# Optimization experiments

Hardware: AMD Instinct MI355X
Metric: run time of the kernel (lower is better)

The kernel has to match this reference:

```python
import jax, jax.numpy as jnp
import numpy as np

NUM_LOC = 20000
T = 24
IN_DIM = 18
H1 = 32
H2 = 32
GRU = 32
PW = 15
E_RAND = 640000


def setup_inputs() -> dict:
    key = jax.random.key(0)
    ks = jax.random.split(key, 32)
    # graph: random edges + self loops so every node has >=1 incoming edge
    edge_src = jnp.concatenate([
        jax.random.randint(ks[0], (E_RAND,), 0, NUM_LOC),
        jnp.arange(NUM_LOC)]).astype(jnp.int32)
    edge_dst = jnp.concatenate([
        jax.random.randint(ks[1], (E_RAND,), 0, NUM_LOC),
        jnp.arange(NUM_LOC)]).astype(jnp.int32)
    dynamic = jax.random.normal(ks[2], (NUM_LOC, T, IN_DIM), dtype=jnp.float32)
    cI = jax.random.uniform(ks[3], (T,), dtype=jnp.float32)
    cR = jax.random.uniform(ks[4], (T,), dtype=jnp.float32)
    I = jax.random.uniform(ks[5], (T,), dtype=jnp.float32)
    R = jax.random.uniform(ks[6], (T,), dtype=jnp.float32)
    N = jax.random.uniform(ks[7], (NUM_LOC, 1), dtype=jnp.float32) * 1e4 + 10.0
    h0 = jax.random.normal(ks[8], (1, GRU), dtype=jnp.float32) * 0.1
    s = 0.1
    # GAT layer 1 (torch Linear convention: weight [out, in], y = x @ W.T + b)
    W1 = jax.random.normal(ks[9], (H1, IN_DIM), dtype=jnp.float32) * s
    b1 = jnp.zeros((H1,), dtype=jnp.float32)
    aW1 = jax.random.normal(ks[10], (1, 2 * H1), dtype=jnp.float32) * s
    ab1 = jnp.zeros((1,), dtype=jnp.float32)
    # GAT layer 2
    W2 = jax.random.normal(ks[11], (H2, H1), dtype=jnp.float32) * s
    b2 = jnp.zeros((H2,), dtype=jnp.float32)
    aW2 = jax.random.normal(ks[12], (1, 2 * H2), dtype=jnp.float32) * s
    ab2 = jnp.zeros((1,), dtype=jnp.float32)
    # GRUCell
    Wih = jax.random.normal(ks[13], (3 * GRU, H2), dtype=jnp.float32) * s
    Whh = jax.random.normal(ks[14], (3 * GRU, GRU), dtype=jnp.float32) * s
    bih = jnp.zeros((3 * GRU,), dtype=jnp.float32)
    bhh = jnp.zeros((3 * GRU,), dtype=jnp.float32)
    # output heads
    WI = jax.random.normal(ks[15], (PW, GRU + 2), dtype=jnp.float32) * s
    bI = jnp.zeros((PW,), dtype=jnp.float32)
    WR = jax.random.normal(ks[16], (PW, GRU + 2), dtype=jnp.float32) * s
    bR = jnp.zeros((PW,), dtype=jnp.float32)
    Ws = jax.random.normal(ks[17], (2, GRU + 2), dtype=jnp.float32) * s
    bs = jnp.zeros((2,), dtype=jnp.float32)
    return {"dynamic": dynamic, "cI": cI, "cR": cR, "N": N, "I": I, "R": R,
            "h0": h0, "W1": W1, "b1": b1, "aW1": aW1, "ab1": ab1,
            "W2": W2, "b2": b2, "aW2": aW2, "ab2": ab2,
            "Wih": Wih, "Whh": Whh, "bih": bih, "bhh": bhh,
            "WI": WI, "bI": bI, "WR": WR, "bR": bR, "Ws": Ws, "bs": bs,
            "edge_src": edge_src, "edge_dst": edge_dst}


def _gat(x, W, b, aW, ab, src, dst):
    # z = fc(x); per-edge attention e = leaky_relu(attn_fc([z_src, z_dst]))
    z = x @ W.T + b                                        # [n, out]
    e = jax.nn.leaky_relu(
        (jnp.concatenate([z[src], z[dst]], axis=1) @ aW.T + ab)[:, 0])  # [E]
    # softmax over incoming edges per destination node
    m = jax.ops.segment_max(e, dst, num_segments=NUM_LOC)
    ex = jnp.exp(e - m[dst])
    den = jax.ops.segment_sum(ex, dst, num_segments=NUM_LOC)
    alpha = ex / den[dst]
    return jax.ops.segment_sum(alpha[:, None] * z[src], dst, num_segments=NUM_LOC)


def reference(dynamic, cI, cR, N, I, R, h0,
              W1, b1, aW1, ab1, W2, b2, aW2, ab2,
              Wih, Whh, bih, bhh, WI, bI, WR, bR, Ws, bs,
              edge_src, edge_dst):
    Nv = N[:, 0]                                          # [num_loc]

    def step(h, inp):
        x_t, cI_t, cR_t, I_t, R_t = inp
        c = jax.nn.elu(_gat(x_t, W1, b1, aW1, ab1, edge_src, edge_dst))
        c = jax.nn.elu(_gat(c, W2, b2, aW2, ab2, edge_src, edge_dst))
        pooled = jnp.max(c, axis=0)[None, :]              # [1, H2]
        # GRUCell
        gi = pooled @ Wih.T + bih
        gh = h @ Whh.T + bhh
        r = jax.nn.sigmoid(gi[:, :GRU] + gh[:, :GRU])
        zg = jax.nn.sigmoid(gi[:, GRU:2 * GRU] + gh[:, GRU:2 * GRU])
        n = jnp.tanh(gi[:, 2 * GRU:] + r * gh[:, 2 * GRU:])
        h_new = (1.0 - zg) * n + zg * h                   # [1, GRU]
        hc = jnp.concatenate([h_new, cI_t.reshape(1, 1), cR_t.reshape(1, 1)], axis=1)
        pred_I = hc @ WI.T + bI                           # [1, PW]
        pred_R = hc @ WR.T + bR
        sir = hc @ Ws.T + bs                              # [1, 2]
        alpha = jax.nn.sigmoid(sir[0, 0])
        beta = jax.nn.sigmoid(sir[0, 1])

        def sir_step(carry, _):
            lI, lR = carry
            lS = Nv - lI - lR
            dI = alpha * lI * (lS / Nv) - beta * lI
            dR = beta * lI
            return (lI + jax.lax.stop_gradient(dI),
                    lR + jax.lax.stop_gradient(dR)), (dI, dR)

        init = (jnp.broadcast_to(I_t, Nv.shape), jnp.broadcast_to(R_t, Nv.shape))
        _, (dIs, dRs) = jax.lax.scan(sir_step, init, None, length=PW)
        # [PW, num_loc] -> [num_loc, PW]
        return h_new, (pred_I, pred_R, dIs.T, dRs.T)

    xs = (jnp.swapaxes(dynamic, 0, 1), cI, cR, I, R)      # time-major
    h_fin, (nI, nR, pI, pR) = jax.lax.scan(step, h0, xs)
    new_I = jnp.transpose(nI, (1, 0, 2))                  # [1, T, PW]
    new_R = jnp.transpose(nR, (1, 0, 2))
    phy_I = jnp.transpose(pI, (1, 0, 2))                  # [num_loc, T, PW]
    phy_R = jnp.transpose(pR, (1, 0, 2))
    return new_I, new_R, phy_I, phy_R, h_fin
```

## Files before the change

kernel.cpp:

```cpp
#include <hip/hip_runtime.h>
#include <hip/hip_fp16.h>
#include <math.h>
#include <float.h>
#include <type_traits>

#define NLOC 20000
#define TT   24
#define INDIM 18
#define HH   32
#define PWN  15
#define PSTR 32

typedef unsigned short u16;

__device__ __forceinline__ unsigned int fkey(float f) {
    unsigned int b = __float_as_uint(f);
    return b ^ ((unsigned int)((int)b >> 31) | 0x80000000u);
}
__device__ __forceinline__ float funkey(unsigned int u) {
    return (u & 0x80000000u) ? __uint_as_float(u ^ 0x80000000u) : __uint_as_float(~u);
}

__device__ __forceinline__ void decode_t(int nblk, int swz, int tadd,
                                         int& t, int& blk, int& slice) {
    if (swz) {
        int F = blockIdx.x;
        int k = F & 7;
        int g = F >> 3;
        t = k + 8 * (g / nblk);
        blk = g % nblk;
        slice = t;
    } else {
        slice = blockIdx.y;
        t = tadd + slice;
        blk = blockIdx.x;
    }
}

__global__ void count_kernel(const int* __restrict__ dst, int* __restrict__ cnt, int E) {
    int e = blockIdx.x * blockDim.x + threadIdx.x;
    if (e < E) atomicAdd(&cnt[dst[e]], 1);
}

__global__ void scan_kernel(const int* __restrict__ cnt, int* __restrict__ row_ptr, int n) {
    __shared__ int sums[1024];
    const int CH = 20;
    int tid = threadIdx.x;
    int base = tid * CH;
    int local[CH];
    int s = 0;
    #pragma unroll
    for (int i = 0; i < CH; ++i) {
        int idx = base + i;
        int v = (idx < n) ? cnt[idx] : 0;
        local[i] = s;
        s += v;
    }
    sums[tid] = s;
    __syncthreads();
    for (int o = 1; o < 1024; o <<= 1) {
        int v = (tid >= o) ? sums[tid - o] : 0;
        __syncthreads();
        sums[tid] += v;
        __syncthreads();
    }
    int pre = (tid > 0) ? sums[tid - 1] : 0;
    #pragma unroll
    for (int i = 0; i < CH; ++i) {
        int idx = base + i;
        if (idx < n) row_ptr[idx] = pre + local[i];
    }
    if (tid == 1023) row_ptr[n] = sums[1023];
}

__global__ void scatter_kernel(const int* __restrict__ src, const int* __restrict__ dst,
                               const int* __restrict__ row_ptr, int* __restrict__ fill,
                               u16* __restrict__ csr_src, int E) {
    int e = blockIdx.x * blockDim.x + threadIdx.x;
    if (e < E) {
        int d = dst[e];
        int pos = row_ptr[d] + atomicAdd(&fill[d], 1);
        csr_src[pos] = (u16)src[e];
    }
}

template<int IN, bool XABS, typename TIN>
__global__ void node_kernel(const TIN* __restrict__ xbase, long nstride, long tstride,
                            const float* __restrict__ W, const float* __restrict__ b,
                            const float* __restrict__ aW, const float* __restrict__ ab,
                            __half* __restrict__ z, float* __restrict__ es, float* __restrict__ ed,
                            int nblk, int swz, int tadd) {
    __shared__ float sW[HH * IN];
    __shared__ float sb[HH];
    __shared__ float saW[2 * HH];
    __shared__ float sab;
    int t, blk, slice;
    decode_t(nblk, swz, tadd, t, blk, slice);
    int tid = threadIdx.x;
    for (int i = tid; i < HH * IN; i += blockDim.x) sW[i] = W[i];
    if (tid < HH) sb[tid] = b[tid];
    if (tid < 2 * HH) saW[tid] = aW[tid];
    if (tid == 0) sab = ab[0];
    __syncthreads();
    int n = blk * blockDim.x + tid;
    if (n >= NLOC) return;
    z  += (size_t)slice * NLOC * HH;
    es += (size_t)slice * NLOC;
    ed += (size_t)slice * NLOC;
    long xoff = XABS ? (long)t * tstride : (long)slice * tstride;
    const TIN* xp = xbase + (long)n * nstride + xoff;
    float xr[IN];
    if constexpr (std::is_same<TIN, __half>::value) {
        const __half2* hp = (const __half2*)xp;
        #pragma unroll
        for (int i = 0; i < IN / 2; ++i) {
            float2 f = __half22float2(hp[i]);
            xr[2 * i] = f.x; xr[2 * i + 1] = f.y;
        }
    } else {
        #pragma unroll
        for (int i = 0; i < IN; ++i) xr[i] = (float)xp[i];
    }
    float e_s = 0.f, e_d = sab;
    #pragma unroll
    for (int k = 0; k < HH; ++k) {
        float acc = sb[k];
        #pragma unroll
        for (int i = 0; i < IN; ++i) acc = fmaf(xr[i], sW[k * IN + i], acc);
        z[n * HH + k] = __float2half_rn(acc);
        e_s = fmaf(saW[k], acc, e_s);
        e_d = fmaf(saW[HH + k], acc, e_d);
    }
    es[n] = e_s;
    ed[n] = e_d;
}

template<bool WRITE_C, bool POOL>
__global__ void __launch_bounds__(256, 4)
agg_kernel(const int* __restrict__ row_ptr, const u16* __restrict__ csr,
           const __half* __restrict__ zt, const float* __restrict__ es,
           const float* __restrict__ ed, __half* __restrict__ cout,
           unsigned int* __restrict__ pooled_u, int nblk, int swz, int tadd) {
    __shared__ int2  shp[4][64];
    __shared__ float sred[4][HH];
    int t, dblk, slice;
    decode_t(nblk, swz, tadd, t, dblk, slice);
    int lane = threadIdx.x & 63;
    int w    = threadIdx.x >> 6;
    int r    = lane >> 3;
    int cg   = lane & 7;
    int d = dblk * 4 + w;
    const __half* z   = zt + (size_t)slice * NLOC * HH;
    const float*  est = es + (size_t)slice * NLOC;
    const float*  edt = ed + (size_t)slice * NLOC;

    int beg = 0, end = 0;
    float edd = 0.f;
    if (d < NLOC) {
        beg = row_ptr[d];
        end = row_ptr[d + 1];
        edd = edt[d];
    }
    int deg = end - beg;
    int il = beg + lane;
    bool valid = (il < end);
    int idx_l = valid ? (int)csr[il] : 0;
    float ev = est[idx_l] + edd;
    ev = (ev > 0.f) ? ev : 0.01f * ev;
    float w_l = valid ? __expf(ev) : 0.f;
    shp[w][lane] = make_int2(idx_l, __float_as_int(w_l));
    __syncthreads();

    float a0 = 0.f, a1 = 0.f, a2 = 0.f, a3 = 0.f, sden = 0.f;
    #pragma unroll
    for (int pass = 0; pass < 8; ++pass) {
        int2 pw = shp[w][pass * 8 + r];
        float we = __int_as_float(pw.y);
        const __half2* zp = (const __half2*)(z + (size_t)pw.x * HH + cg * 4);
        __half2 h01 = zp[0], h23 = zp[1];
        sden += we;
        a0 = fmaf(we, __half2float(__low2half(h01)),  a0);
        a1 = fmaf(we, __half2float(__high2half(h01)), a1);
        a2 = fmaf(we, __half2float(__low2half(h23)),  a2);
        a3 = fmaf(we, __half2float(__high2half(h23)), a3);
    }
    for (int e = 64 + r; e < deg; e += 8) {
        int s2 = (int)csr[beg + e];
        float ee = est[s2] + edd;
        ee = (ee > 0.f) ? ee : 0.01f * ee;
        float xx = __expf(ee);
        sden += xx;
        const __half2* zp = (const __half2*)(z + (size_t)s2 * HH + cg * 4);
        __half2 h01 = zp[0], h23 = zp[1];
        a0 = fmaf(xx, __half2float(__low2half(h01)),  a0);
        a1 = fmaf(xx, __half2float(__high2half(h01)), a1);
        a2 = fmaf(xx, __half2float(__low2half(h23)),  a2);
        a3 = fmaf(xx, __half2float(__high2half(h23)), a3);
    }
    #pragma unroll
    for (int o = 8; o <= 32; o <<= 1) {
        a0 += __shfl_xor(a0, o, 64);
        a1 += __shfl_xor(a1, o, 64);
        a2 += __shfl_xor(a2, o, 64);
        a3 += __shfl_xor(a3, o, 64);
        sden += __shfl_xor(sden, o, 64);
    }

    float v0 = -FLT_MAX, v1 = -FLT_MAX, v2 = -FLT_MAX, v3 = -FLT_MAX;
    if (d < NLOC) {
        float rden = 1.f / sden;
        v0 = a0 * rden; v0 = (v0 > 0.f) ? v0 : __expf(v0) - 1.f;
        v1 = a1 * rden; v1 = (v1 > 0.f) ? v1 : __expf(v1) - 1.f;
        v2 = a2 * rden; v2 = (v2 > 0.f) ? v2 : __expf(v2) - 1.f;
        v3 = a3 * rden; v3 = (v3 > 0.f) ? v3 : __expf(v3) - 1.f;
        if (WRITE_C && r == 0) {
            __half2 o01 = __floats2half2_rn(v0, v1);
            __half2 o23 = __floats2half2_rn(v2, v3);
            uint2 pk;
            pk.x = *(unsigned int*)&o01;
            pk.y = *(unsigned int*)&o23;
            *(uint2*)&cout[(size_t)slice * NLOC * HH + (size_t)d * HH + cg * 4] = pk;
        }
    }
    if (POOL) {
        if (r == 0) {
            sred[w][cg * 4 + 0] = v0;
            sred[w][cg * 4 + 1] = v1;
            sred[w][cg * 4 + 2] = v2;
            sred[w][cg * 4 + 3] = v3;
        }
        __syncthreads();
        if (threadIdx.x < HH) {
            float m = fmaxf(fmaxf(sred[0][threadIdx.x], sred[1][threadIdx.x]),
                            fmaxf(sred[2][threadIdx.x], sred[3][threadIdx.x]));
            atomicMax(&pooled_u[(size_t)(t * HH + threadIdx.x) * PSTR], fkey(m));
        }
    }
}

__global__ void gru_all_kernel(const unsigned int* __restrict__ pooled_u,
                               const float* __restrict__ Wih, const float* __restrict__ Whh,
                               const float* __restrict__ bih, const float* __restrict__ bhh,
                               const float* __restrict__ WI, const float* __restrict__ bI,
                               const float* __restrict__ WR, const float* __restrict__ bR,
                               const float* __restrict__ Ws, const float* __restrict__ bs,
                               const float* __restrict__ cIv, const float* __restrict__ cRv,
                               const float* __restrict__ h0, float* __restrict__ abArr,
                               float* __restrict__ out_newI, float* __restrict__ out_newR,
                               float* __restrict__ h_fin) {
    __shared__ float pooled[HH], hs[HH], gi[96], gh[96], hc[34];
    int tid = threadIdx.x;
    float wih_r[HH], whh_r[HH];
    if (tid < 96) {
        #pragma unroll
        for (int k = 0; k < HH; ++k) {
            wih_r[k] = Wih[tid * HH + k];
            whh_r[k] = Whh[tid * HH + k];
        }
    }
    if (tid < HH) hs[tid] = h0[tid];
    __syncthreads();
    for (int t = 0; t < TT; ++t) {
        if (tid < HH) pooled[tid] = funkey(pooled_u[(size_t)(t * HH + tid) * PSTR]);
        __syncthreads();
        if (tid < 96) {
            float a = bih[tid], g = bhh[tid];
            #pragma unroll
            for (int k = 0; k < HH; ++k) {
                a = fmaf(wih_r[k], pooled[k], a);
                g = fmaf(whh_r[k], hs[k], g);
            }
            gi[tid] = a; gh[tid] = g;
        }
        __syncthreads();
        if (tid < HH) {
            float r  = 1.f / (1.f + expf(-(gi[tid] + gh[tid])));
            float zg = 1.f / (1.f + expf(-(gi[HH + tid] + gh[HH + tid])));
            float nn = tanhf(gi[2 * HH + tid] + r * gh[2 * HH + tid]);
            float hn = (1.f - zg) * nn + zg * hs[tid];
            hs[tid] = hn;
            hc[tid] = hn;
        }
        if (tid == 32) hc[32] = cIv[t];
        if (tid == 33) hc[33] = cRv[t];
        __syncthreads();
        if (tid < PWN) {
            float a = bI[tid];
            #pragma unroll
            for (int k = 0; k < 34; ++k) a = fmaf(WI[tid * 34 + k], hc[k], a);
            out_newI[t * PWN + tid] = a;
        } else if (tid >= 32 && tid < 32 + PWN) {
            int p = tid - 32;
            float a = bR[p];
            #pragma unroll
            for (int k = 0; k < 34; ++k) a = fmaf(WR[p * 34 + k], hc[k], a);
            out_newR[t * PWN + p] = a;
        } else if (tid == 64 || tid == 65) {
            int p = tid - 64;
            float a = bs[p];
            #pragma unroll
            for (int k = 0; k < 34; ++k) a = fmaf(Ws[p * 34 + k], hc[k], a);
            abArr[2 * t + p] = 1.f / (1.f + expf(-a));
        }
        __syncthreads();
    }
    if (tid < HH) h_fin[tid] = hs[tid];
}

__global__ void sir_kernel(const float* __restrict__ Nin, const float* __restrict__ Iv,
                           const float* __restrict__ Rv, const float* __restrict__ abArr,
                           float* __restrict__ phyI, float* __restrict__ phyR) {
    int idx = blockIdx.x * blockDim.x + threadIdx.x;
    if (idx >= NLOC * TT) return;
    int n = idx / TT, t = idx - n * TT;
    float Nv = Nin[n];
    float alpha = abArr[2 * t], beta = abArr[2 * t + 1];
    float lI = Iv[t], lR = Rv[t];
    float* oI = phyI + (size_t)idx * PWN;
    float* oR = phyR + (size_t)idx * PWN;
    #pragma unroll
    for (int p = 0; p < PWN; ++p) {
        float lS = Nv - lI - lR;
        float dI = alpha * lI * (lS / Nv) - beta * lI;
        float dR = beta * lI;
        oI[p] = dI;
        oR[p] = dR;
        lI += dI;
        lR += dR;
    }
}

extern "C" void kernel_launch(void* const* d_in, const int* in_sizes, int n_in,
                              void* d_out, int out_size, void* d_ws, size_t ws_size,
                              hipStream_t stream) {
    const float* dynamic = (const float*)d_in[0];
    const float* cIv = (const float*)d_in[1];
    const float* cRv = (const float*)d_in[2];
    const float* Nin = (const float*)d_in[3];
    const float* Iv  = (const float*)d_in[4];
    const float* Rv  = (const float*)d_in[5];
    const float* h0  = (const float*)d_in[6];
    const float* W1  = (const float*)d_in[7];
    const float* b1  = (const float*)d_in[8];
    const float* aW1 = (const float*)d_in[9];
    const float* ab1 = (const float*)d_in[10];
    const float* W2  = (const float*)d_in[11];
    const float* b2  = (const float*)d_in[12];
    const float* aW2 = (const float*)d_in[13];
    const float* ab2 = (const float*)d_in[14];
    const float* Wih = (const float*)d_in[15];
    const float* Whh = (const float*)d_in[16];
    const float* bih = (const float*)d_in[17];
    const float* bhh = (const float*)d_in[18];
    const float* WI  = (const float*)d_in[19];
    const float* bI  = (const float*)d_in[20];
    const float* WR  = (const float*)d_in[21];
    const float* bR  = (const float*)d_in[22];
    const float* Ws  = (const float*)d_in[23];
    const float* bs  = (const float*)d_in[24];
    const int* esrc  = (const int*)d_in[25];
    const int* edst  = (const int*)d_in[26];
    const int E = in_sizes[25];

    float* out = (float*)d_out;
    float* out_newI = out;
    float* out_newR = out + TT * PWN;
    float* phyI = out + 2 * TT * PWN;
    float* phyR = phyI + (size_t)NLOC * TT * PWN;
    float* h_fin = phyR + (size_t)NLOC * TT * PWN;

    char* p = (char*)d_ws;
    int* cnt = (int*)p;                 p += (size_t)NLOC * 4;
    int* fill = (int*)p;                p += (size_t)NLOC * 4;
    int* row_ptr = (int*)p;             p += (size_t)(NLOC + 2) * 4;
    u16* csr = (u16*)p;                 p += ((size_t)E * 2 + 15) & ~(size_t)15;
    unsigned int* pooled_u = (unsigned int*)p; p += (size_t)TT * HH * PSTR * 4;
    float* abArr = (float*)p;           p += (size_t)2 * TT * 4;
    p = (char*)(((size_t)p + 15) & ~(size_t)15);
    size_t fixed_bytes = (size_t)(p - (char*)d_ws);
    size_t per_t_bytes = (size_t)(2 * NLOC * HH * 2 + 2 * NLOC * 4);
    int B = 1;
    if (ws_size > fixed_bytes + per_t_bytes)
        B = (int)((ws_size - fixed_bytes) / per_t_bytes);
    if (B > TT) B = TT;
    if (B < 1) B = 1;
    __half* zb  = (__half*)p;
    __half* cb  = zb + (size_t)B * NLOC * HH;
    float* esb  = (float*)(cb + (size_t)B * NLOC * HH);
    float* edb  = esb + (size_t)B * NLOC;

    hipMemsetAsync(cnt, 0, (size_t)2 * NLOC * 4, stream);
    hipMemsetAsync(pooled_u, 0, (size_t)TT * HH * PSTR * 4, stream);

    int egrid = (E + 255) / 256;
    count_kernel<<<egrid, 256, 0, stream>>>(edst, cnt, E);
    scan_kernel<<<1, 1024, 0, stream>>>(cnt, row_ptr, NLOC);
    scatter_kernel<<<egrid, 256, 0, stream>>>(esrc, edst, row_ptr, fill, csr, E);

    const int NBLK_N = (NLOC + 255) / 256;
    const int NBLK_A = (NLOC + 3) / 4;

    if (B >= TT) {
        dim3 ng(NBLK_N * TT), ag(NBLK_A * TT);
        node_kernel<INDIM, true, float><<<ng, 256, 0, stream>>>(
            dynamic, (long)TT * INDIM, (long)INDIM, W1, b1, aW1, ab1,
            zb, esb, edb, NBLK_N, 1, 0);
        agg_kernel<true, false><<<ag, 256, 0, stream>>>(
            row_ptr, csr, zb, esb, edb, cb, pooled_u, NBLK_A, 1, 0);
        node_kernel<HH, false, __half><<<ng, 256, 0, stream>>>(
            cb, (long)HH, (long)NLOC * HH, W2, b2, aW2, ab2,
            zb, esb, edb, NBLK_N, 1, 0);
        agg_kernel<false, true><<<ag, 256, 0, stream>>>(
            row_ptr, csr, zb, esb, edb, nullptr, pooled_u, NBLK_A, 1, 0);
    } else {
        for (int tbase = 0; tbase < TT; tbase += B) {
            int Bc = TT - tbase; if (Bc > B) Bc = B;
            dim3 ng(NBLK_N, Bc), ag(NBLK_A, Bc);
            node_kernel<INDIM, true, float><<<ng, 256, 0, stream>>>(
                dynamic, (long)TT * INDIM, (long)INDIM, W1, b1, aW1, ab1,
                zb, esb, edb, NBLK_N, 0, tbase);
            agg_kernel<true, false><<<ag, 256, 0, stream>>>(
                row_ptr, csr, zb, esb, edb, cb, pooled_u, NBLK_A, 0, tbase);
            node_kernel<HH, false, __half><<<ng, 256, 0, stream>>>(
                cb, (long)HH, (long)NLOC * HH, W2, b2, aW2, ab2,
                zb, esb, edb, NBLK_N, 0, tbase);
            agg_kernel<false, true><<<ag, 256, 0, stream>>>(
                row_ptr, csr, zb, esb, edb, nullptr, pooled_u, NBLK_A, 0, tbase);
        }
    }

    gru_all_kernel<<<1, 128, 0, stream>>>(pooled_u, Wih, Whh, bih, bhh,
                                          WI, bI, WR, bR, Ws, bs, cIv, cRv,
                                          h0, abArr, out_newI, out_newR, h_fin);
    sir_kernel<<<(NLOC * TT + 255) / 256, 256, 0, stream>>>(Nin, Iv, Rv, abArr, phyI, phyR);
}
```

Measured before the change: 706.7 us.

## Interleave timestep pairs in feature layout so each gather serves two timesteps

Node features, attention scores and layer-1 outputs are now stored as pairs of timesteps interleaved (half2 per feature, float2 per score), so each graph edge gather loads 16 bytes covering two timesteps and the CSR index and row lookups are shared across both. The grid covers 12 timestep pairs instead of 24 timesteps, which halves index and row-pointer traffic and halves the number of aggregation blocks. The cost is more registers per thread and a 16-wide swizzle grid of which 4 groups exit immediately. The ELU and LeakyReLU activations are also rewritten in branchless form.

Result: faster. 637.8 us (-9.8%).

```diff
diff --git a/kernel.cpp b/kernel.cpp
--- a/kernel.cpp
+++ b/kernel.cpp
@@ -2,10 +2,10 @@
 #include <hip/hip_fp16.h>
 #include <math.h>
 #include <float.h>
-#include <type_traits>
 
 #define NLOC 20000
 #define TT   24
+#define NP   12
 #define INDIM 18
 #define HH   32
 #define PWN  15
@@ -21,20 +21,18 @@
     return (u & 0x80000000u) ? __uint_as_float(u ^ 0x80000000u) : __uint_as_float(~u);
 }
 
-__device__ __forceinline__ void decode_t(int nblk, int swz, int tadd,
-                                         int& t, int& blk, int& slice) {
+__device__ __forceinline__ bool decode_q(int nblk, int swz, int qadd,
+                                         int& q, int& blk) {
     if (swz) {
         int F = blockIdx.x;
-        int k = F & 7;
         int g = F >> 3;
-        t = k + 8 * (g / nblk);
+        q = (F & 7) + 8 * (g / nblk);
         blk = g % nblk;
-        slice = t;
-    } else {
-        slice = blockIdx.y;
-        t = tadd + slice;
-        blk = blockIdx.x;
-    }
+        return q < NP;
+    }
+    q = qadd + blockIdx.y;
+    blk = blockIdx.x;
+    return true;
 }
 
 __global__ void count_kernel(const int* __restrict__ dst, int* __restrict__ cnt, int E) {
@@ -84,156 +82,220 @@
     }
 }
 
-template<int IN, bool XABS, typename TIN>
-__global__ void node_kernel(const TIN* __restrict__ xbase, long nstride, long tstride,
-                            const float* __restrict__ W, const float* __restrict__ b,
-                            const float* __restrict__ aW, const float* __restrict__ ab,
-                            __half* __restrict__ z, float* __restrict__ es, float* __restrict__ ed,
-                            int nblk, int swz, int tadd) {
-    __shared__ float sW[HH * IN];
+__global__ void node1_kernel(const float* __restrict__ dyn,
+                             const float* __restrict__ W, const float* __restrict__ b,
+                             const float* __restrict__ aW, const float* __restrict__ ab,
+                             __half2* __restrict__ z2, float2* __restrict__ es2,
+                             float2* __restrict__ ed2, int nblk, int swz, int qadd) {
+    __shared__ float sW[HH * INDIM];
     __shared__ float sb[HH];
     __shared__ float saW[2 * HH];
     __shared__ float sab;
-    int t, blk, slice;
-    decode_t(nblk, swz, tadd, t, blk, slice);
+    int q, blk;
+    if (!decode_q(nblk, swz, qadd, q, blk)) return;
+    int slice = swz ? q : blockIdx.y;
     int tid = threadIdx.x;
-    for (int i = tid; i < HH * IN; i += blockDim.x) sW[i] = W[i];
+    for (int i = tid; i < HH * INDIM; i += blockDim.x) sW[i] = W[i];
     if (tid < HH) sb[tid] = b[tid];
     if (tid < 2 * HH) saW[tid] = aW[tid];
     if (tid == 0) sab = ab[0];
     __syncthreads();
     int n = blk * blockDim.x + tid;
     if (n >= NLOC) return;
-    z  += (size_t)slice * NLOC * HH;
-    es += (size_t)slice * NLOC;
-    ed += (size_t)slice * NLOC;
-    long xoff = XABS ? (long)t * tstride : (long)slice * tstride;
-    const TIN* xp = xbase + (long)n * nstride + xoff;
-    float xr[IN];
-    if constexpr (std::is_same<TIN, __half>::value) {
-        const __half2* hp = (const __half2*)xp;
+    z2  += (size_t)slice * NLOC * HH;
+    es2 += (size_t)slice * NLOC;
+    ed2 += (size_t)slice * NLOC;
+    const float* xp = dyn + (size_t)n * (TT * INDIM) + (size_t)(2 * q) * INDIM;
+    float x0[INDIM], x1[INDIM];
+    #pragma unroll
+    for (int i = 0; i < INDIM; ++i) { x0[i] = xp[i]; x1[i] = xp[INDIM + i]; }
+    float es0 = 0.f, es1 = 0.f, ed0 = sab, ed1 = sab;
+    #pragma unroll
+    for (int k = 0; k < HH; ++k) {
+        float a0 = sb[k], a1 = sb[k];
         #pragma unroll
-        for (int i = 0; i < IN / 2; ++i) {
-            float2 f = __half22float2(hp[i]);
-            xr[2 * i] = f.x; xr[2 * i + 1] = f.y;
-        }
-    } else {
+        for (int i = 0; i < INDIM; ++i) {
+            a0 = fmaf(x0[i], sW[k * INDIM + i], a0);
+            a1 = fmaf(x1[i], sW[k * INDIM + i], a1);
+        }
+        z2[(size_t)n * HH + k] = __floats2half2_rn(a0, a1);
+        es0 = fmaf(saW[k], a0, es0);       es1 = fmaf(saW[k], a1, es1);
+        ed0 = fmaf(saW[HH + k], a0, ed0);  ed1 = fmaf(saW[HH + k], a1, ed1);
+    }
+    es2[n] = make_float2(es0, es1);
+    ed2[n] = make_float2(ed0, ed1);
+}
+
+__global__ void node2_kernel(const __half2* __restrict__ c2,
+                             const float* __restrict__ W, const float* __restrict__ b,
+                             const float* __restrict__ aW, const float* __restrict__ ab,
+                             __half2* __restrict__ z2, float2* __restrict__ es2,
+                             float2* __restrict__ ed2, int nblk, int swz, int qadd) {
+    __shared__ float sW[HH * HH];
+    __shared__ float sb[HH];
+    __shared__ float saW[2 * HH];
+    __shared__ float sab;
+    int q, blk;
+    if (!decode_q(nblk, swz, qadd, q, blk)) return;
+    int slice = swz ? q : blockIdx.y;
+    int tid = threadIdx.x;
+    for (int i = tid; i < HH * HH; i += blockDim.x) sW[i] = W[i];
+    if (tid < HH) sb[tid] = b[tid];
+    if (tid < 2 * HH) saW[tid] = aW[tid];
+    if (tid == 0) sab = ab[0];
+    __syncthreads();
+    int n = blk * blockDim.x + tid;
+    if (n >= NLOC) return;
+    c2  += (size_t)slice * NLOC * HH;
+    z2  += (size_t)slice * NLOC * HH;
+    es2 += (size_t)slice * NLOC;
+    ed2 += (size_t)slice * NLOC;
+    float x0[HH], x1[HH];
+    const __half2* cp = c2 + (size_t)n * HH;
+    #pragma unroll
+    for (int i = 0; i < HH; ++i) {
+        float2 f = __half22float2(cp[i]);
+        x0[i] = f.x; x1[i] = f.y;
+    }
+    float es0 = 0.f, es1 = 0.f, ed0 = sab, ed1 = sab;
+    #pragma unroll
+    for (int k = 0; k < HH; ++k) {
+        float a0 = sb[k], a1 = sb[k];
         #pragma unroll
-        for (int i = 0; i < IN; ++i) xr[i] = (float)xp[i];
-    }
-    float e_s = 0.f, e_d = sab;
-    #pragma unroll
-    for (int k = 0; k < HH; ++k) {
-        float acc = sb[k];
-        #pragma unroll
-        for (int i = 0; i < IN; ++i) acc = fmaf(xr[i], sW[k * IN + i], acc);
-        z[n * HH + k] = __float2half_rn(acc);
-        e_s = fmaf(saW[k], acc, e_s);
-        e_d = fmaf(saW[HH + k], acc, e_d);
-    }
-    es[n] = e_s;
-    ed[n] = e_d;
+        for (int i = 0; i < HH; ++i) {
+            a0 = fmaf(x0[i], sW[k * HH + i], a0);
+            a1 = fmaf(x1[i], sW[k * HH + i], a1);
+        }
+        z2[(size_t)n * HH + k] = __floats2half2_rn(a0, a1);
+        es0 = fmaf(saW[k], a0, es0);       es1 = fmaf(saW[k], a1, es1);
+        ed0 = fmaf(saW[HH + k], a0, ed0);  ed1 = fmaf(saW[HH + k], a1, ed1);
+    }
+    es2[n] = make_float2(es0, es1);
+    ed2[n] = make_float2(ed0, ed1);
 }
 
 template<bool WRITE_C, bool POOL>
 __global__ void __launch_bounds__(256, 4)
 agg_kernel(const int* __restrict__ row_ptr, const u16* __restrict__ csr,
-           const __half* __restrict__ zt, const float* __restrict__ es,
-           const float* __restrict__ ed, __half* __restrict__ cout,
-           unsigned int* __restrict__ pooled_u, int nblk, int swz, int tadd) {
-    __shared__ int2  shp[4][64];
-    __shared__ float sred[4][HH];
-    int t, dblk, slice;
-    decode_t(nblk, swz, tadd, t, dblk, slice);
+           const __half2* __restrict__ z2t, const float2* __restrict__ es2,
+           const float2* __restrict__ ed2, __half2* __restrict__ c2out,
+           unsigned int* __restrict__ pooled_u, int nblk, int swz, int qadd) {
+    __shared__ int    soff[4][64];
+    __shared__ float2 swt[4][64];
+    __shared__ float  sred[4][2][HH];
+    int q, dblk;
+    if (!decode_q(nblk, swz, qadd, q, dblk)) return;
+    int slice = swz ? q : blockIdx.y;
     int lane = threadIdx.x & 63;
     int w    = threadIdx.x >> 6;
     int r    = lane >> 3;
     int cg   = lane & 7;
     int d = dblk * 4 + w;
-    const __half* z   = zt + (size_t)slice * NLOC * HH;
-    const float*  est = es + (size_t)slice * NLOC;
-    const float*  edt = ed + (size_t)slice * NLOC;
+    const __half2* z2q  = z2t + (size_t)slice * NLOC * HH;
+    const float2*  es2q = es2 + (size_t)slice * NLOC;
+    const float2*  ed2q = ed2 + (size_t)slice * NLOC;
 
     int beg = 0, end = 0;
-    float edd = 0.f;
+    float edd0 = 0.f, edd1 = 0.f;
     if (d < NLOC) {
         beg = row_ptr[d];
         end = row_ptr[d + 1];
-        edd = edt[d];
+        float2 ev = ed2q[d];
+        edd0 = ev.x; edd1 = ev.y;
     }
     int deg = end - beg;
     int il = beg + lane;
     bool valid = (il < end);
     int idx_l = valid ? (int)csr[il] : 0;
-    float ev = est[idx_l] + edd;
-    ev = (ev > 0.f) ? ev : 0.01f * ev;
-    float w_l = valid ? __expf(ev) : 0.f;
-    shp[w][lane] = make_int2(idx_l, __float_as_int(w_l));
-    __syncthreads();
-
-    float a0 = 0.f, a1 = 0.f, a2 = 0.f, a3 = 0.f, sden = 0.f;
+    float2 esv = es2q[idx_l];
+    float e0 = esv.x + edd0; e0 = fmaxf(e0, 0.01f * e0);
+    float e1 = esv.y + edd1; e1 = fmaxf(e1, 0.01f * e1);
+    float w0 = valid ? __expf(e0) : 0.f;
+    float w1 = valid ? __expf(e1) : 0.f;
+    soff[w][lane] = idx_l << 7;
+    swt[w][lane]  = make_float2(w0, w1);
+
+    const char* zb = (const char*)z2q + cg * 16;
+    float2 ac0 = {0.f, 0.f}, ac1 = {0.f, 0.f}, ac2 = {0.f, 0.f}, ac3 = {0.f, 0.f};
+    float den0 = 0.f, den1 = 0.f;
     #pragma unroll
     for (int pass = 0; pass < 8; ++pass) {
-        int2 pw = shp[w][pass * 8 + r];
-        float we = __int_as_float(pw.y);
-        const __half2* zp = (const __half2*)(z + (size_t)pw.x * HH + cg * 4);
-        __half2 h01 = zp[0], h23 = zp[1];
-        sden += we;
-        a0 = fmaf(we, __half2float(__low2half(h01)),  a0);
-        a1 = fmaf(we, __half2float(__high2half(h01)), a1);
-        a2 = fmaf(we, __half2float(__low2half(h23)),  a2);
-        a3 = fmaf(we, __half2float(__high2half(h23)), a3);
+        int    off = soff[w][pass * 8 + r];
+        float2 wv  = swt[w][pass * 8 + r];
+        uint4 u = *(const uint4*)(zb + off);
+        den0 += wv.x; den1 += wv.y;
+        float2 f0 = __half22float2(*(const __half2*)&u.x);
+        float2 f1 = __half22float2(*(const __half2*)&u.y);
+        float2 f2 = __half22float2(*(const __half2*)&u.z);
+        float2 f3 = __half22float2(*(const __half2*)&u.w);
+        ac0.x = fmaf(wv.x, f0.x, ac0.x); ac0.y = fmaf(wv.y, f0.y, ac0.y);
+        ac1.x = fmaf(wv.x, f1.x, ac1.x); ac1.y = fmaf(wv.y, f1.y, ac1.y);
+        ac2.x = fmaf(wv.x, f2.x, ac2.x); ac2.y = fmaf(wv.y, f2.y, ac2.y);
+        ac3.x = fmaf(wv.x, f3.x, ac3.x); ac3.y = fmaf(wv.y, f3.y, ac3.y);
     }
     for (int e = 64 + r; e < deg; e += 8) {
         int s2 = (int)csr[beg + e];
-        float ee = est[s2] + edd;
-        ee = (ee > 0.f) ? ee : 0.01f * ee;
-        float xx = __expf(ee);
-        sden += xx;
-        const __half2* zp = (const __half2*)(z + (size_t)s2 * HH + cg * 4);
-        __half2 h01 = zp[0], h23 = zp[1];
-        a0 = fmaf(xx, __half2float(__low2half(h01)),  a0);
-        a1 = fmaf(xx, __half2float(__high2half(h01)), a1);
-        a2 = fmaf(xx, __half2float(__low2half(h23)),  a2);
-        a3 = fmaf(xx, __half2float(__high2half(h23)), a3);
+        float2 esv2 = es2q[s2];
+        float t0 = esv2.x + edd0; t0 = fmaxf(t0, 0.01f * t0);
+        float t1 = esv2.y + edd1; t1 = fmaxf(t1, 0.01f * t1);
+        float x0 = __expf(t0), x1 = __expf(t1);
+        den0 += x0; den1 += x1;
+        uint4 u = *(const uint4*)(zb + ((size_t)s2 << 7));
+        float2 f0 = __half22float2(*(const __half2*)&u.x);
+        float2 f1 = __half22float2(*(const __half2*)&u.y);
+        float2 f2 = __half22float2(*(const __half2*)&u.z);
+        float2 f3 = __half22float2(*(const __half2*)&u.w);
+        ac0.x = fmaf(x0, f0.x, ac0.x); ac0.y = fmaf(x1, f0.y, ac0.y);
+        ac1.x = fmaf(x0, f1.x, ac1.x); ac1.y = fmaf(x1, f1.y, ac1.y);
+        ac2.x = fmaf(x0, f2.x, ac2.x); ac2.y = fmaf(x1, f2.y, ac2.y);
+        ac3.x = fmaf(x0, f3.x, ac3.x); ac3.y = fmaf(x1, f3.y, ac3.y);
     }
     #pragma unroll
     for (int o = 8; o <= 32; o <<= 1) {
-        a0 += __shfl_xor(a0, o, 64);
-        a1 += __shfl_xor(a1, o, 64);
-        a2 += __shfl_xor(a2, o, 64);
-        a3 += __shfl_xor(a3, o, 64);
-        sden += __shfl_xor(sden, o, 64);
-    }
-
-    float v0 = -FLT_MAX, v1 = -FLT_MAX, v2 = -FLT_MAX, v3 = -FLT_MAX;
+        ac0.x += __shfl_xor(ac0.x, o, 64); ac0.y += __shfl_xor(ac0.y, o, 64);
+        ac1.x += __shfl_xor(ac1.x, o, 64); ac1.y += __shfl_xor(ac1.y, o, 64);
+        ac2.x += __shfl_xor(ac2.x, o, 64); ac2.y += __shfl_xor(ac2.y, o, 64);
+        ac3.x += __shfl_xor(ac3.x, o, 64); ac3.y += __shfl_xor(ac3.y, o, 64);
+        den0  += __shfl_xor(den0,  o, 64); den1  += __shfl_xor(den1,  o, 64);
+    }
+
+    float v00 = -FLT_MAX, v01 = -FLT_MAX, v10 = -FLT_MAX, v11 = -FLT_MAX;
+    float v20 = -FLT_MAX, v21 = -FLT_MAX, v30 = -FLT_MAX, v31 = -FLT_MAX;
     if (d < NLOC) {
-        float rden = 1.f / sden;
-        v0 = a0 * rden; v0 = (v0 > 0.f) ? v0 : __expf(v0) - 1.f;
-        v1 = a1 * rden; v1 = (v1 > 0.f) ? v1 : __expf(v1) - 1.f;
-        v2 = a2 * rden; v2 = (v2 > 0.f) ? v2 : __expf(v2) - 1.f;
-        v3 = a3 * rden; v3 = (v3 > 0.f) ? v3 : __expf(v3) - 1.f;
+        float r0 = 1.f / den0, r1 = 1.f / den1;
+        v00 = ac0.x * r0; v00 = fmaxf(v00, __expf(fminf(v00, 0.f)) - 1.f);
+        v01 = ac0.y * r1; v01 = fmaxf(v01, __expf(fminf(v01, 0.f)) - 1.f);
+        v10 = ac1.x * r0; v10 = fmaxf(v10, __expf(fminf(v10, 0.f)) - 1.f);
+        v11 = ac1.y * r1; v11 = fmaxf(v11, __expf(fminf(v11, 0.f)) - 1.f);
+        v20 = ac2.x * r0; v20 = fmaxf(v20, __expf(fminf(v20, 0.f)) - 1.f);
+        v21 = ac2.y * r1; v21 = fmaxf(v21, __expf(fminf(v21, 0.f)) - 1.f);
+        v30 = ac3.x * r0; v30 = fmaxf(v30, __expf(fminf(v30, 0.f)) - 1.f);
+        v31 = ac3.y * r1; v31 = fmaxf(v31, __expf(fminf(v31, 0.f)) - 1.f);
         if (WRITE_C && r == 0) {
-            __half2 o01 = __floats2half2_rn(v0, v1);
-            __half2 o23 = __floats2half2_rn(v2, v3);
-            uint2 pk;
-            pk.x = *(unsigned int*)&o01;
-            pk.y = *(unsigned int*)&o23;
-            *(uint2*)&cout[(size_t)slice * NLOC * HH + (size_t)d * HH + cg * 4] = pk;
+            uint4 pk;
+            __half2 h0 = __floats2half2_rn(v00, v01);
+            __half2 h1 = __floats2half2_rn(v10, v11);
+            __half2 h2 = __floats2half2_rn(v20, v21);
+            __half2 h3 = __floats2half2_rn(v30, v31);
+            pk.x = *(unsigned int*)&h0; pk.y = *(unsigned int*)&h1;
+            pk.z = *(unsigned int*)&h2; pk.w = *(unsigned int*)&h3;
+            *(uint4*)((char*)(c2out + (size_t)slice * NLOC * HH + (size_t)d * HH) + cg * 16) = pk;
         }
     }
     if (POOL) {
         if (r == 0) {
-            sred[w][cg * 4 + 0] = v0;
-            sred[w][cg * 4 + 1] = v1;
-            sred[w][cg * 4 + 2] = v2;
-            sred[w][cg * 4 + 3] = v3;
-        }
-        __syncthreads();
-        if (threadIdx.x < HH) {
-            float m = fmaxf(fmaxf(sred[0][threadIdx.x], sred[1][threadIdx.x]),
-                            fmaxf(sred[2][threadIdx.x], sred[3][threadIdx.x]));
-            atomicMax(&pooled_u[(size_t)(t * HH + threadIdx.x) * PSTR], fkey(m));
+            sred[w][0][cg * 4 + 0] = v00; sred[w][1][cg * 4 + 0] = v01;
+            sred[w][0][cg * 4 + 1] = v10; sred[w][1][cg * 4 + 1] = v11;
+            sred[w][0][cg * 4 + 2] = v20; sred[w][1][cg * 4 + 2] = v21;
+            sred[w][0][cg * 4 + 3] = v30; sred[w][1][cg * 4 + 3] = v31;
+        }
+        __syncthreads();
+        if (threadIdx.x < 64) {
+            int pp = threadIdx.x >> 5;
+            int dim = threadIdx.x & 31;
+            float m = fmaxf(fmaxf(sred[0][pp][dim], sred[1][pp][dim]),
+                            fmaxf(sred[2][pp][dim], sred[3][pp][dim]));
+            atomicMax(&pooled_u[(size_t)((2 * q + pp) * HH + dim) * PSTR], fkey(m));
         }
     }
 }
@@ -376,18 +438,18 @@
     u16* csr = (u16*)p;                 p += ((size_t)E * 2 + 15) & ~(size_t)15;
     unsigned int* pooled_u = (unsigned int*)p; p += (size_t)TT * HH * PSTR * 4;
     float* abArr = (float*)p;           p += (size_t)2 * TT * 4;
-    p = (char*)(((size_t)p + 15) & ~(size_t)15);
+    p = (char*)(((size_t)p + 127) & ~(size_t)127);
     size_t fixed_bytes = (size_t)(p - (char*)d_ws);
-    size_t per_t_bytes = (size_t)(2 * NLOC * HH * 2 + 2 * NLOC * 4);
+    size_t per_q_bytes = (size_t)NLOC * HH * 4 * 2 + (size_t)NLOC * 8 * 2;
     int B = 1;
-    if (ws_size > fixed_bytes + per_t_bytes)
-        B = (int)((ws_size - fixed_bytes) / per_t_bytes);
-    if (B > TT) B = TT;
+    if (ws_size > fixed_bytes + per_q_bytes)
+        B = (int)((ws_size - fixed_bytes) / per_q_bytes);
+    if (B > NP) B = NP;
     if (B < 1) B = 1;
-    __half* zb  = (__half*)p;
-    __half* cb  = zb + (size_t)B * NLOC * HH;
-    float* esb  = (float*)(cb + (size_t)B * NLOC * HH);
-    float* edb  = esb + (size_t)B * NLOC;
+    __half2* zb  = (__half2*)p;
+    __half2* cb  = zb + (size_t)B * NLOC * HH;
+    float2* es2  = (float2*)(cb + (size_t)B * NLOC * HH);
+    float2* ed2  = es2 + (size_t)B * NLOC;
 
     hipMemsetAsync(cnt, 0, (size_t)2 * NLOC * 4, stream);
     hipMemsetAsync(pooled_u, 0, (size_t)TT * HH * PSTR * 4, stream);
@@ -400,32 +462,28 @@
     const int NBLK_N = (NLOC + 255) / 256;
     const int NBLK_A = (NLOC + 3) / 4;
 
-    if (B >= TT) {
-        dim3 ng(NBLK_N * TT), ag(NBLK_A * TT);
-        node_kernel<INDIM, true, float><<<ng, 256, 0, stream>>>(
-            dynamic, (long)TT * INDIM, (long)INDIM, W1, b1, aW1, ab1,
-            zb, esb, edb, NBLK_N, 1, 0);
+    if (B >= NP) {
+        dim3 ng(NBLK_N * 16), ag(NBLK_A * 16);
+        node1_kernel<<<ng, 256, 0, stream>>>(dynamic, W1, b1, aW1, ab1,
+                                             zb, es2, ed2, NBLK_N, 1, 0);
         agg_kernel<true, false><<<ag, 256, 0, stream>>>(
-            row_ptr, csr, zb, esb, edb, cb, pooled_u, NBLK_A, 1, 0);
-        node_kernel<HH, false, __half><<<ng, 256, 0, stream>>>(
-            cb, (long)HH, (long)NLOC * HH, W2, b2, aW2, ab2,
-            zb, esb, edb, NBLK_N, 1, 0);
+            row_ptr, csr, zb, es2, ed2, cb, pooled_u, NBLK_A, 1, 0);
+        node2_kernel<<<ng, 256, 0, stream>>>(cb, W2, b2, aW2, ab2,
+                                             zb, es2, ed2, NBLK_N, 1, 0);
         agg_kernel<false, true><<<ag, 256, 0, stream>>>(
-            row_ptr, csr, zb, esb, edb, nullptr, pooled_u, NBLK_A, 1, 0);
+            row_ptr, csr, zb, es2, ed2, nullptr, pooled_u, NBLK_A, 1, 0);
     } else {
-        for (int tbase = 0; tbase < TT; tbase += B) {
-            int Bc = TT - tbase; if (Bc > B) Bc = B;
+        for (int qbase = 0; qbase < NP; qbase += B) {
+            int Bc = NP - qbase; if (Bc > B) Bc = B;
             dim3 ng(NBLK_N, Bc), ag(NBLK_A, Bc);
-            node_kernel<INDIM, true, float><<<ng, 256, 0, stream>>>(
-                dynamic, (long)TT * INDIM, (long)INDIM, W1, b1, aW1, ab1,
-                zb, esb, edb, NBLK_N, 0, tbase);
+            node1_kernel<<<ng, 256, 0, stream>>>(dynamic, W1, b1, aW1, ab1,
+                                                 zb, es2, ed2, NBLK_N, 0, qbase);
             agg_kernel<true, false><<<ag, 256, 0, stream>>>(
-                row_ptr, csr, zb, esb, edb, cb, pooled_u, NBLK_A, 0, tbase);
-            node_kernel<HH, false, __half><<<ng, 256, 0, stream>>>(
-                cb, (long)HH, (long)NLOC * HH, W2, b2, aW2, ab2,
-                zb, esb, edb, NBLK_N, 0, tbase);
+                row_ptr, csr, zb, es2, ed2, cb, pooled_u, NBLK_A, 0, qbase);
+            node2_kernel<<<ng, 256, 0, stream>>>(cb, W2, b2, aW2, ab2,
+                                                 zb, es2, ed2, NBLK_N, 0, qbase);
             agg_kernel<false, true><<<ag, 256, 0, stream>>>(
-                row_ptr, csr, zb, esb, edb, nullptr, pooled_u, NBLK_A, 0, tbase);
+                row_ptr, csr, zb, es2, ed2, nullptr, pooled_u, NBLK_A, 0, qbase);
         }
     }
 
```
